# Performance work log

Measured on AMD Instinct MI355X. Metric: run time of the kernel, lower is better.

## Reference

```python
import jax, jax.numpy as jnp
import numpy as np

TOKENS = 8192
IN_F = 4096
OUT_F = 4096
ZERO_POINT = 0  # int8 activation zero point (module default)


def setup_inputs() -> dict:
    key = jax.random.key(0)
    k1, k2, k3, k4 = jax.random.split(key, 4)
    # int8-valued activations/weights stored as int32 (same math as torch upcast path)
    x = jax.random.randint(k1, (TOKENS, IN_F), 0, 127, dtype=jnp.int32)
    weight = jax.random.randint(k2, (IN_F, OUT_F), -127, 127, dtype=jnp.int32)
    bias = jax.random.randint(k3, (1, OUT_F), -64, 64, dtype=jnp.int32)
    gemm_scales = jax.random.uniform(k4, (1, OUT_F), dtype=jnp.float32) * 1e-3
    return {"x": x, "weight": weight, "bias": bias, "gemm_scales": gemm_scales}


def reference(x, weight, bias, gemm_scales):
    # adjust_a = (x - zero_point), upcast to float32 like the torch module
    adjust_a = (x - ZERO_POINT).astype(jnp.float32)          # [T, in]
    w = weight.astype(jnp.float32)                           # [in, out]
    gemm_o = (adjust_a @ w + bias.astype(jnp.float32)) * gemm_scales  # [T, out]
    return gemm_o
```

## Files before the change

### kernel.cpp

```cpp
#include <hip/hip_runtime.h>

using i32x4 = __attribute__((ext_vector_type(4))) int;

#define AS3(p) ((__attribute__((address_space(3))) void*)(p))
#define AS1(p) ((const __attribute__((address_space(1))) void*)(p))

constexpr int M = 8192;
constexpr int N = 4096;
constexpr int K = 4096;
constexpr int BK = 64;
constexpr int NT = K / BK;
constexpr int NBUF = 4;

__global__ void pack_a_kernel(const int4* __restrict__ x, unsigned* __restrict__ a8, int nUnits) {
    int stride = gridDim.x * blockDim.x;
    for (int u = blockIdx.x * blockDim.x + threadIdx.x; u < nUnits; u += stride) {
        int4 v = x[u];
        a8[u] = (v.x & 255) | ((v.y & 255) << 8) | ((v.z & 255) << 16) | (v.w << 24);
    }
}

__global__ void pack_wT_kernel(const int* __restrict__ w, char* __restrict__ b8t) {
    __shared__ __align__(16) char T[64][80];
    const int n0 = blockIdx.x * 64;
    const int k0 = blockIdx.y * 64;
    const int tid = threadIdx.x;

    #pragma unroll
    for (int i = 0; i < 4; i++) {
        int u = tid + i * 256;
        int r = u >> 4;
        int c = u & 15;
        int4 v = *(const int4*)&w[(size_t)(k0 + r) * N + n0 + 4 * c];
        T[4 * c + 0][r] = (char)v.x;
        T[4 * c + 1][r] = (char)v.y;
        T[4 * c + 2][r] = (char)v.z;
        T[4 * c + 3][r] = (char)v.w;
    }
    __syncthreads();

    const int n = tid >> 2;
    const int q = tid & 3;
    int4 val = *(const int4*)&T[n][16 * q];
    *(int4*)&b8t[(size_t)(n0 + n) * K + k0 + 16 * q] = val;
}

__global__ __launch_bounds__(512, 2) void gemm_i8_kernel(
    const char* __restrict__ a8, const char* __restrict__ b8t,
    const int* __restrict__ bias, const float* __restrict__ scales,
    float* __restrict__ out)
{
    __shared__ __align__(16) char As[NBUF][256 * BK];
    __shared__ __align__(16) char Bs[NBUF][256 * BK];

    const int tid  = threadIdx.x;
    const int lane = tid & 63;
    const int wid  = tid >> 6;
    const int wr   = wid >> 2;
    const int wc   = wid & 3;

    const int bid = blockIdx.x;
    const int xcd = bid & 7;
    const int l   = bid >> 3;
    const int tm  = (xcd >> 1) * 8 + (l >> 3);
    const int tn  = (xcd & 1) * 8 + (l & 7);
    const size_t brow = (size_t)tm * 256;
    const size_t bcol = (size_t)tn * 256;

    const int srow = tid >> 2;
    const int schS = ((tid & 3) ^ ((tid >> 3) & 3)) << 4;
    const char* aG = a8  + (brow + srow) * (size_t)K + schS;
    const char* bG = b8t + (bcol + srow) * (size_t)K + schS;
    const int ldsW = wid * 1024;

    i32x4 acc[8][4];
    #pragma unroll
    for (int m = 0; m < 8; m++)
        #pragma unroll
        for (int n = 0; n < 4; n++)
            #pragma unroll
            for (int r = 0; r < 4; r++)
                acc[m][n][r] = 0;

    auto stage = [&](int slot, int kt) {
        const char* a = aG + (size_t)kt * BK;
        const char* b = bG + (size_t)kt * BK;
        char* Ad = &As[slot][0] + ldsW;
        char* Bd = &Bs[slot][0] + ldsW;
        __builtin_amdgcn_global_load_lds(AS1(a),                  AS3(Ad),        16, 0, 0);
        __builtin_amdgcn_global_load_lds(AS1(a + (size_t)128*K),  AS3(Ad + 8192), 16, 0, 0);
        __builtin_amdgcn_global_load_lds(AS1(b),                  AS3(Bd),        16, 0, 0);
        __builtin_amdgcn_global_load_lds(AS1(b + (size_t)128*K),  AS3(Bd + 8192), 16, 0, 0);
    };

    const int frow  = lane & 15;
    const int c0sw  = ((lane >> 4) ^ ((frow >> 1) & 3)) << 4;
    const int raOff = wr * 8192 + frow * 64 + c0sw;
    const int rbOff = wc * 4096 + frow * 64 + c0sw;

    stage(0, 0);
    stage(1, 1);
    stage(2, 2);
    asm volatile("s_waitcnt vmcnt(8)" ::: "memory");
    __builtin_amdgcn_s_barrier();

    for (int t = 0; t < NT; ++t) {
        const int slot = t & 3;
        if (t + 3 < NT) stage((t + 3) & 3, t + 3);

        const char* Ab = &As[slot][0] + raOff;
        const char* Bb = &Bs[slot][0] + rbOff;

        i32x4 bfr[4];
        #pragma unroll
        for (int n = 0; n < 4; ++n)
            bfr[n] = *(const i32x4*)(Bb + n * 1024);

        i32x4 aCur = *(const i32x4*)(Ab);
        __builtin_amdgcn_s_setprio(1);
        #pragma unroll
        for (int m = 0; m < 8; ++m) {
            i32x4 aNext;
            if (m < 7) aNext = *(const i32x4*)(Ab + (m + 1) * 1024);
            #pragma unroll
            for (int n = 0; n < 4; ++n)
                acc[m][n] = __builtin_amdgcn_mfma_i32_16x16x64_i8(aCur, bfr[n], acc[m][n], 0, 0, 0);
            aCur = aNext;
        }
        __builtin_amdgcn_s_setprio(0);

        if (t <= NT - 4) asm volatile("s_waitcnt vmcnt(8)" ::: "memory");
        else             asm volatile("s_waitcnt vmcnt(0)" ::: "memory");
        __builtin_amdgcn_s_barrier();
    }

    #pragma unroll
    for (int n = 0; n < 4; ++n) {
        const int col = (int)bcol + wc * 64 + n * 16 + (lane & 15);
        const int bv  = bias[col];
        const float sv = scales[col];
        #pragma unroll
        for (int m = 0; m < 8; ++m) {
            const size_t row0 = brow + wr * 128 + m * 16 + ((lane >> 4) << 2);
            float* o = out + row0 * (size_t)N + col;
            #pragma unroll
            for (int r = 0; r < 4; ++r)
                o[(size_t)r * N] = (float)(acc[m][n][r] + bv) * sv;
        }
    }
}

extern "C" void kernel_launch(void* const* d_in, const int* in_sizes, int n_in,
                              void* d_out, int out_size, void* d_ws, size_t ws_size,
                              hipStream_t stream) {
    const int*   x      = (const int*)d_in[0];
    const int*   w      = (const int*)d_in[1];
    const int*   bias   = (const int*)d_in[2];
    const float* scales = (const float*)d_in[3];
    float* out = (float*)d_out;

    char* a8  = (char*)d_ws;
    char* b8t = a8 + (size_t)M * K;

    pack_a_kernel<<<2048, 256, 0, stream>>>((const int4*)x, (unsigned*)a8, M * K / 4);

    dim3 gt(N / 64, K / 64);
    pack_wT_kernel<<<gt, 256, 0, stream>>>(w, b8t);

    gemm_i8_kernel<<<(M / 256) * (N / 256), 512, 0, stream>>>(a8, b8t, bias, scales, out);
}
```

Baseline: 240.2 us.

## Double-buffer LDS fragments in registers and deepen global prefetch to four stages

```diff
diff --git a/kernel.cpp b/kernel.cpp
--- a/kernel.cpp
+++ b/kernel.cpp
@@ -98,40 +98,51 @@
     const int raOff = wr * 8192 + frow * 64 + c0sw;
     const int rbOff = wc * 4096 + frow * 64 + c0sw;
 
-    stage(0, 0);
-    stage(1, 1);
-    stage(2, 2);
+    i32x4 fAa[8], fAb[4], fBa[8], fBb[4];
+
+    stage(0, 0); stage(1, 1); stage(2, 2); stage(3, 3);
     asm volatile("s_waitcnt vmcnt(8)" ::: "memory");
     __builtin_amdgcn_s_barrier();
+    {
+        const char* Ab = &As[0][0] + raOff;
+        const char* Bb = &Bs[0][0] + rbOff;
+        #pragma unroll
+        for (int n = 0; n < 4; ++n) fAb[n] = *(const i32x4*)(Bb + n * 1024);
+        #pragma unroll
+        for (int m = 0; m < 8; ++m) fAa[m] = *(const i32x4*)(Ab + m * 1024);
+    }
+    asm volatile("s_waitcnt lgkmcnt(0)" ::: "memory");
+    __builtin_amdgcn_s_barrier();
 
-    for (int t = 0; t < NT; ++t) {
-        const int slot = t & 3;
-        if (t + 3 < NT) stage((t + 3) & 3, t + 3);
-
-        const char* Ab = &As[slot][0] + raOff;
-        const char* Bb = &Bs[slot][0] + rbOff;
-
-        i32x4 bfr[4];
-        #pragma unroll
-        for (int n = 0; n < 4; ++n)
-            bfr[n] = *(const i32x4*)(Bb + n * 1024);
-
-        i32x4 aCur = *(const i32x4*)(Ab);
+    auto body = [&](int t, i32x4 (&cA)[8], i32x4 (&cB)[4], i32x4 (&nA)[8], i32x4 (&nB)[4]) {
+        if (t + 4 < NT) stage(t & 3, t + 4);
+        if (t + 1 < NT) {
+            const int slot = (t + 1) & 3;
+            const char* Ab = &As[slot][0] + raOff;
+            const char* Bb = &Bs[slot][0] + rbOff;
+            #pragma unroll
+            for (int n = 0; n < 4; ++n) nB[n] = *(const i32x4*)(Bb + n * 1024);
+            #pragma unroll
+            for (int m = 0; m < 8; ++m) nA[m] = *(const i32x4*)(Ab + m * 1024);
+        }
+        __builtin_amdgcn_sched_barrier(0);
         __builtin_amdgcn_s_setprio(1);
         #pragma unroll
-        for (int m = 0; m < 8; ++m) {
-            i32x4 aNext;
-            if (m < 7) aNext = *(const i32x4*)(Ab + (m + 1) * 1024);
+        for (int m = 0; m < 8; ++m)
             #pragma unroll
             for (int n = 0; n < 4; ++n)
-                acc[m][n] = __builtin_amdgcn_mfma_i32_16x16x64_i8(aCur, bfr[n], acc[m][n], 0, 0, 0);
-            aCur = aNext;
-        }
+                acc[m][n] = __builtin_amdgcn_mfma_i32_16x16x64_i8(cA[m], cB[n], acc[m][n], 0, 0, 0);
         __builtin_amdgcn_s_setprio(0);
+        asm volatile("s_waitcnt lgkmcnt(0)" ::: "memory");
+        if (t < NT - 4)       asm volatile("s_waitcnt vmcnt(8)" ::: "memory");
+        else if (t == NT - 4) asm volatile("s_waitcnt vmcnt(4)" ::: "memory");
+        else                  asm volatile("s_waitcnt vmcnt(0)" ::: "memory");
+        __builtin_amdgcn_s_barrier();
+    };
 
-        if (t <= NT - 4) asm volatile("s_waitcnt vmcnt(8)" ::: "memory");
-        else             asm volatile("s_waitcnt vmcnt(0)" ::: "memory");
-        __builtin_amdgcn_s_barrier();
+    for (int t = 0; t < NT; t += 2) {
+        body(t,     fAa, fAb, fBa, fBb);
+        body(t + 1, fBa, fBb, fAa, fAb);
     }
 
     #pragma unroll
```

Result: faster. 229.8 us (-4.3%).

## Shrink GEMM tile to 256x128 with triple buffering for higher occupancy

Applied to the files above, without the earlier changes.

```diff
diff --git a/kernel.cpp b/kernel.cpp
--- a/kernel.cpp
+++ b/kernel.cpp
@@ -8,9 +8,11 @@
 constexpr int M = 8192;
 constexpr int N = 4096;
 constexpr int K = 4096;
+constexpr int BM = 256;
+constexpr int BN = 128;
 constexpr int BK = 64;
 constexpr int NT = K / BK;
-constexpr int NBUF = 4;
+constexpr int NBUF = 3;
 
 __global__ void pack_a_kernel(const int4* __restrict__ x, unsigned* __restrict__ a8, int nUnits) {
     int stride = gridDim.x * blockDim.x;
@@ -45,37 +47,37 @@
     *(int4*)&b8t[(size_t)(n0 + n) * K + k0 + 16 * q] = val;
 }
 
-__global__ __launch_bounds__(512, 2) void gemm_i8_kernel(
+__global__ __launch_bounds__(512, 4) void gemm_i8_kernel(
     const char* __restrict__ a8, const char* __restrict__ b8t,
     const int* __restrict__ bias, const float* __restrict__ scales,
     float* __restrict__ out)
 {
-    __shared__ __align__(16) char As[NBUF][256 * BK];
-    __shared__ __align__(16) char Bs[NBUF][256 * BK];
+    __shared__ __align__(16) char As[NBUF][BM * BK];
+    __shared__ __align__(16) char Bs[NBUF][BN * BK];
 
     const int tid  = threadIdx.x;
     const int lane = tid & 63;
     const int wid  = tid >> 6;
-    const int wr   = wid >> 2;
-    const int wc   = wid & 3;
+    const int wr   = wid >> 1;
+    const int wc   = wid & 1;
 
     const int bid = blockIdx.x;
     const int xcd = bid & 7;
     const int l   = bid >> 3;
-    const int tm  = (xcd >> 1) * 8 + (l >> 3);
-    const int tn  = (xcd & 1) * 8 + (l & 7);
-    const size_t brow = (size_t)tm * 256;
-    const size_t bcol = (size_t)tn * 256;
+    const int tm  = (xcd >> 1) * 8 + (l >> 4);
+    const int tn  = (xcd & 1) * 16 + (l & 15);
+    const size_t brow = (size_t)tm * BM;
+    const size_t bcol = (size_t)tn * BN;
 
     const int srow = tid >> 2;
     const int schS = ((tid & 3) ^ ((tid >> 3) & 3)) << 4;
-    const char* aG = a8  + (brow + srow) * (size_t)K + schS;
-    const char* bG = b8t + (bcol + srow) * (size_t)K + schS;
+    const char* aGs = a8  + (brow + srow) * (size_t)K + schS;
+    const char* bGs = b8t + (bcol + srow) * (size_t)K + schS;
     const int ldsW = wid * 1024;
 
-    i32x4 acc[8][4];
+    i32x4 acc[4][4];
     #pragma unroll
-    for (int m = 0; m < 8; m++)
+    for (int m = 0; m < 4; m++)
         #pragma unroll
         for (int n = 0; n < 4; n++)
             #pragma unroll
@@ -83,55 +85,53 @@
                 acc[m][n][r] = 0;
 
     auto stage = [&](int slot, int kt) {
-        const char* a = aG + (size_t)kt * BK;
-        const char* b = bG + (size_t)kt * BK;
-        char* Ad = &As[slot][0] + ldsW;
-        char* Bd = &Bs[slot][0] + ldsW;
-        __builtin_amdgcn_global_load_lds(AS1(a),                  AS3(Ad),        16, 0, 0);
-        __builtin_amdgcn_global_load_lds(AS1(a + (size_t)128*K),  AS3(Ad + 8192), 16, 0, 0);
-        __builtin_amdgcn_global_load_lds(AS1(b),                  AS3(Bd),        16, 0, 0);
-        __builtin_amdgcn_global_load_lds(AS1(b + (size_t)128*K),  AS3(Bd + 8192), 16, 0, 0);
+        const char* a = aGs + (size_t)kt * BK;
+        const char* b = bGs + (size_t)kt * BK;
+        __builtin_amdgcn_global_load_lds(AS1(a),                  AS3(&As[slot][ldsW]),        16, 0, 0);
+        __builtin_amdgcn_global_load_lds(AS1(a + (size_t)128*K),  AS3(&As[slot][8192 + ldsW]), 16, 0, 0);
+        __builtin_amdgcn_global_load_lds(AS1(b),                  AS3(&Bs[slot][ldsW]),        16, 0, 0);
     };
 
-    const int frow  = lane & 15;
-    const int c0sw  = ((lane >> 4) ^ ((frow >> 1) & 3)) << 4;
-    const int raOff = wr * 8192 + frow * 64 + c0sw;
+    const int frow = lane & 15;
+    const int c0sw = ((lane >> 4) ^ ((frow >> 1) & 3)) << 4;
+    const int raOff = wr * 4096 + frow * 64 + c0sw;
     const int rbOff = wc * 4096 + frow * 64 + c0sw;
 
     stage(0, 0);
     stage(1, 1);
-    stage(2, 2);
-    asm volatile("s_waitcnt vmcnt(8)" ::: "memory");
+    asm volatile("s_waitcnt vmcnt(3)" ::: "memory");
     __builtin_amdgcn_s_barrier();
 
+    int s = 0;
     for (int t = 0; t < NT; ++t) {
-        const int slot = t & 3;
-        if (t + 3 < NT) stage((t + 3) & 3, t + 3);
+        int sp = s - 1; if (sp < 0) sp = 2;
+        const bool more = (t + 2 < NT);
+        if (more) stage(sp, t + 2);
 
-        const char* Ab = &As[slot][0] + raOff;
-        const char* Bb = &Bs[slot][0] + rbOff;
+        const char* Ab = &As[s][0] + raOff;
+        const char* Bb = &Bs[s][0] + rbOff;
 
         i32x4 bfr[4];
         #pragma unroll
         for (int n = 0; n < 4; ++n)
             bfr[n] = *(const i32x4*)(Bb + n * 1024);
 
-        i32x4 aCur = *(const i32x4*)(Ab);
         __builtin_amdgcn_s_setprio(1);
         #pragma unroll
-        for (int m = 0; m < 8; ++m) {
-            i32x4 aNext;
-            if (m < 7) aNext = *(const i32x4*)(Ab + (m + 1) * 1024);
+        for (int m = 0; m < 4; ++m) {
+            i32x4 af = *(const i32x4*)(Ab + m * 1024);
             #pragma unroll
             for (int n = 0; n < 4; ++n)
-                acc[m][n] = __builtin_amdgcn_mfma_i32_16x16x64_i8(aCur, bfr[n], acc[m][n], 0, 0, 0);
-            aCur = aNext;
+                acc[m][n] = __builtin_amdgcn_mfma_i32_16x16x64_i8(af, bfr[n], acc[m][n], 0, 0, 0);
         }
         __builtin_amdgcn_s_setprio(0);
 
-        if (t <= NT - 4) asm volatile("s_waitcnt vmcnt(8)" ::: "memory");
-        else             asm volatile("s_waitcnt vmcnt(0)" ::: "memory");
+        asm volatile("s_waitcnt lgkmcnt(0)" ::: "memory");
+        if (more) asm volatile("s_waitcnt vmcnt(3)" ::: "memory");
+        else      asm volatile("s_waitcnt vmcnt(0)" ::: "memory");
         __builtin_amdgcn_s_barrier();
+
+        s = (s == 2) ? 0 : s + 1;
     }
 
     #pragma unroll
@@ -140,8 +140,8 @@
         const int bv  = bias[col];
         const float sv = scales[col];
         #pragma unroll
-        for (int m = 0; m < 8; ++m) {
-            const size_t row0 = brow + wr * 128 + m * 16 + ((lane >> 4) << 2);
+        for (int m = 0; m < 4; ++m) {
+            const size_t row0 = brow + wr * 64 + m * 16 + ((lane >> 4) << 2);
             float* o = out + row0 * (size_t)N + col;
             #pragma unroll
             for (int r = 0; r < 4; ++r)
@@ -167,5 +167,5 @@
     dim3 gt(N / 64, K / 64);
     pack_wT_kernel<<<gt, 256, 0, stream>>>(w, b8t);
 
-    gemm_i8_kernel<<<(M / 256) * (N / 256), 512, 0, stream>>>(a8, b8t, bias, scales, out);
+    gemm_i8_kernel<<<(M / BM) * (N / BN), 512, 0, stream>>>(a8, b8t, bias, scales, out);
 }
```

Result: faster. 209.1 us (-13.0%).

## Load B fragments directly into registers and shrink A LDS ring to three

Applied to the files above, without the earlier changes.

```diff
diff --git a/kernel.cpp b/kernel.cpp
--- a/kernel.cpp
+++ b/kernel.cpp
@@ -10,7 +10,7 @@
 constexpr int K = 4096;
 constexpr int BK = 64;
 constexpr int NT = K / BK;
-constexpr int NBUF = 4;
+constexpr int NBUF = 3;
 
 __global__ void pack_a_kernel(const int4* __restrict__ x, unsigned* __restrict__ a8, int nUnits) {
     int stride = gridDim.x * blockDim.x;
@@ -51,7 +51,6 @@
     float* __restrict__ out)
 {
     __shared__ __align__(16) char As[NBUF][256 * BK];
-    __shared__ __align__(16) char Bs[NBUF][256 * BK];
 
     const int tid  = threadIdx.x;
     const int lane = tid & 63;
@@ -69,9 +68,10 @@
 
     const int srow = tid >> 2;
     const int schS = ((tid & 3) ^ ((tid >> 3) & 3)) << 4;
-    const char* aG = a8  + (brow + srow) * (size_t)K + schS;
-    const char* bG = b8t + (bcol + srow) * (size_t)K + schS;
+    const char* aGs = a8 + (brow + srow) * (size_t)K + schS;
     const int ldsW = wid * 1024;
+
+    const char* bBase = b8t + (bcol + wc * 64 + (lane & 15)) * (size_t)K + ((lane >> 4) << 4);
 
     i32x4 acc[8][4];
     #pragma unroll
@@ -83,55 +83,54 @@
                 acc[m][n][r] = 0;
 
     auto stage = [&](int slot, int kt) {
-        const char* a = aG + (size_t)kt * BK;
-        const char* b = bG + (size_t)kt * BK;
-        char* Ad = &As[slot][0] + ldsW;
-        char* Bd = &Bs[slot][0] + ldsW;
-        __builtin_amdgcn_global_load_lds(AS1(a),                  AS3(Ad),        16, 0, 0);
-        __builtin_amdgcn_global_load_lds(AS1(a + (size_t)128*K),  AS3(Ad + 8192), 16, 0, 0);
-        __builtin_amdgcn_global_load_lds(AS1(b),                  AS3(Bd),        16, 0, 0);
-        __builtin_amdgcn_global_load_lds(AS1(b + (size_t)128*K),  AS3(Bd + 8192), 16, 0, 0);
+        const char* a = aGs + (size_t)kt * BK;
+        __builtin_amdgcn_global_load_lds(AS1(a),                 AS3(&As[slot][ldsW]),        16, 0, 0);
+        __builtin_amdgcn_global_load_lds(AS1(a + (size_t)128*K), AS3(&As[slot][8192 + ldsW]), 16, 0, 0);
+    };
+    auto loadB = [&](i32x4 (&dst)[4], int kt) {
+        #pragma unroll
+        for (int n = 0; n < 4; ++n)
+            dst[n] = *(const i32x4*)(bBase + (size_t)n * 16 * K + (size_t)kt * BK);
     };
 
-    const int frow  = lane & 15;
-    const int c0sw  = ((lane >> 4) ^ ((frow >> 1) & 3)) << 4;
+    const int frow = lane & 15;
+    const int c0sw = ((lane >> 4) ^ ((frow >> 1) & 3)) << 4;
     const int raOff = wr * 8192 + frow * 64 + c0sw;
-    const int rbOff = wc * 4096 + frow * 64 + c0sw;
 
+    i32x4 bA[4], bB[4];
+
+    loadB(bA, 0);
     stage(0, 0);
     stage(1, 1);
-    stage(2, 2);
-    asm volatile("s_waitcnt vmcnt(8)" ::: "memory");
+    asm volatile("s_waitcnt vmcnt(2)" ::: "memory");
     __builtin_amdgcn_s_barrier();
 
-    for (int t = 0; t < NT; ++t) {
-        const int slot = t & 3;
-        if (t + 3 < NT) stage((t + 3) & 3, t + 3);
+    int s0 = 0;
+    auto body = [&](int t, i32x4 (&bC)[4], i32x4 (&bN)[4]) {
+        int sp = s0 + 2; if (sp >= 3) sp -= 3;
+        if (t + 2 < NT) stage(sp, t + 2);
+        if (t + 1 < NT) loadB(bN, t + 1);
+        asm volatile("s_waitcnt vmcnt(6)" ::: "memory");
 
-        const char* Ab = &As[slot][0] + raOff;
-        const char* Bb = &Bs[slot][0] + rbOff;
-
-        i32x4 bfr[4];
-        #pragma unroll
-        for (int n = 0; n < 4; ++n)
-            bfr[n] = *(const i32x4*)(Bb + n * 1024);
-
-        i32x4 aCur = *(const i32x4*)(Ab);
+        const char* Ab = &As[s0][0] + raOff;
         __builtin_amdgcn_s_setprio(1);
         #pragma unroll
         for (int m = 0; m < 8; ++m) {
-            i32x4 aNext;
-            if (m < 7) aNext = *(const i32x4*)(Ab + (m + 1) * 1024);
+            i32x4 af = *(const i32x4*)(Ab + m * 1024);
             #pragma unroll
             for (int n = 0; n < 4; ++n)
-                acc[m][n] = __builtin_amdgcn_mfma_i32_16x16x64_i8(aCur, bfr[n], acc[m][n], 0, 0, 0);
-            aCur = aNext;
+                acc[m][n] = __builtin_amdgcn_mfma_i32_16x16x64_i8(af, bC[n], acc[m][n], 0, 0, 0);
         }
         __builtin_amdgcn_s_setprio(0);
 
-        if (t <= NT - 4) asm volatile("s_waitcnt vmcnt(8)" ::: "memory");
-        else             asm volatile("s_waitcnt vmcnt(0)" ::: "memory");
+        asm volatile("s_waitcnt lgkmcnt(0)" ::: "memory");
         __builtin_amdgcn_s_barrier();
+        s0 = (s0 == 2) ? 0 : s0 + 1;
+    };
+
+    for (int t = 0; t < NT; t += 2) {
+        body(t,     bA, bB);
+        body(t + 1, bB, bA);
     }
 
     #pragma unroll
```

Result: slower. 268.1 us (+11.6%).
